# Optimization experiments

Hardware: AMD Instinct MI355X
Metric: run time of the kernel (lower is better)

Reference implementation:

```python
import jax, jax.numpy as jnp
import numpy as np


def _d2(a, b):
    # squared euclidean distances, clamped at 0 (matches _full_cdist before sqrt)
    a2 = jnp.sum(a * a, axis=1)[:, None]
    b2 = jnp.sum(b * b, axis=1)[None, :]
    return jnp.clip(a2 + b2 - 2.0 * (a @ b.T), 0.0, None)


def _node_weights(pts, w1, b1, w2, b2):
    h = jax.nn.relu(pts @ w1 + b1)
    logits = h @ w2 + b2
    w = jax.nn.softplus(logits) + 1e-6
    w = w / jnp.sum(w)
    return w[:, 0]


def setup_inputs() -> dict:
    key = jax.random.key(0)
    ks = jax.random.split(key, 8)
    N, M, D, H, S = 8192, 8192, 2, 32, 3
    return {
        "base_points": jax.random.normal(ks[0], (N, D), jnp.float32),
        "target_points": jax.random.normal(ks[1], (M, D), jnp.float32),
        "log_sigmas": jnp.log(jnp.array([0.05, 0.1, 0.2], jnp.float32)),
        "log_scale": 0.1 * jax.random.normal(ks[2], (D,), jnp.float32),
        "wn_w1": jax.random.normal(ks[3], (D, H), jnp.float32) / np.sqrt(D),
        "wn_b1": jnp.zeros((H,), jnp.float32),
        "wn_w2": jax.random.normal(ks[4], (H, 1), jnp.float32) / np.sqrt(H),
        "wn_b2": jnp.zeros((1,), jnp.float32),
        "g_w1": jax.random.normal(ks[5], (4, H), jnp.float32) / 2.0,
        "g_b1": jnp.zeros((H,), jnp.float32),
        "g_w2": jax.random.normal(ks[6], (H, S), jnp.float32) / np.sqrt(H),
        "g_b2": jnp.zeros((S,), jnp.float32),
        "bias": jnp.zeros((1,), jnp.float32),
    }


def reference(base_points, target_points, log_sigmas, log_scale,
              wn_w1, wn_b1, wn_w2, wn_b2,
              g_w1, g_b1, g_w2, g_b2, bias):
    # learned anisotropic per-axis scale
    scale = jnp.exp(log_scale)
    base = base_points * scale
    target = target_points * scale

    # learned positive, normalized node weights (shared weight_net)
    w_b = _node_weights(base, wn_w1, wn_b1, wn_w2, wn_b2)
    w_t = _node_weights(target, wn_w1, wn_b1, wn_w2, wn_b2)

    # kde_mmd_loss with center=True: subtract weighted mean of each cloud.
    bc = base - jnp.sum(w_b[:, None] * base, axis=0)
    tc = target - jnp.sum(w_t[:, None] * target, axis=0)

    # squared distances computed ONCE, reused across all sigma bands
    d2_aa = _d2(bc, bc)
    d2_bb = _d2(tc, tc)
    d2_ab = _d2(bc, tc)

    sigmas = jnp.exp(log_sigmas)

    def band_loss(sigma):
        inv = 1.0 / (2.0 * sigma * sigma)
        kaa = jnp.exp(-d2_aa * inv)
        kbb = jnp.exp(-d2_bb * inv)
        kab = jnp.exp(-d2_ab * inv)
        # weighted MMD^2: w_a K_aa w_a + w_b K_bb w_b - 2 w_a K_ab w_b
        return (w_b @ (kaa @ w_b) + w_t @ (kbb @ w_t)
                - 2.0 * (w_b @ (kab @ w_t)))

    per_band = jnp.stack([band_loss(sigmas[i]) for i in range(sigmas.shape[0])])

    # gating statistics (torch.tensor([...]) detaches -> stop_gradient)
    dist = jnp.sqrt(_d2(base, target))
    mean_dist = jnp.mean(dist)
    var_dist = jnp.var(dist, ddof=1)  # torch .var() is unbiased
    n_base = base_points.shape[0]
    size_diff = abs(float(n_base - target_points.shape[0])) / (n_base + 1e-6)
    weight_var = jnp.var(w_b, ddof=1) + jnp.var(w_t, ddof=1)
    stats = jax.lax.stop_gradient(
        jnp.stack([mean_dist, var_dist,
                   jnp.asarray(size_diff, base.dtype), weight_var]))

    mix_logits = jax.nn.relu(stats @ g_w1 + g_b1) @ g_w2 + g_b2
    gw = jax.nn.softplus(mix_logits)
    gw = gw / jnp.sum(gw)
    return jnp.sum(gw * per_band) + bias[0]
```

## Files before the change

kernel.cpp:

```cpp
#include <hip/hip_runtime.h>
#include <math.h>

#define JT 64
#define ITILE 1024
#define T8 8
#define NJOB_AB 1024
#define NJOB_TRI 576
#define NBLK (NJOB_AB + 2 * NJOB_TRI)
#define L2E 1.4426950408889634f

typedef float v2f __attribute__((ext_vector_type(2)));

__device__ inline float fexp2n(float x) {
  float r;
  asm("v_exp_f32 %0, -%1" : "=v"(r) : "v"(x));
  return r;
}
__device__ inline float fsqrt(float x) {
  float r;
  asm("v_sqrt_f32 %0, %1" : "=v"(r) : "v"(x));
  return r;
}
__device__ inline v2f pk_add(v2f a, v2f b) {
  v2f d;
  asm("v_pk_add_f32 %0, %1, %2" : "=v"(d) : "v"(a), "v"(b));
  return d;
}
__device__ inline v2f pk_mul(v2f a, v2f b) {
  v2f d;
  asm("v_pk_mul_f32 %0, %1, %2" : "=v"(d) : "v"(a), "v"(b));
  return d;
}
__device__ inline v2f pk_fma(v2f a, v2f b, v2f c) {
  v2f d;
  asm("v_pk_fma_f32 %0, %1, %2, %3" : "=v"(d) : "v"(a), "v"(b), "v"(c));
  return d;
}

__device__ inline double wred_d(double v) {
#pragma unroll
  for (int o = 32; o > 0; o >>= 1) v += __shfl_down(v, o, 64);
  return v;
}

__device__ inline double bred(double v, double* sm) {
  v = wred_d(v);
  __syncthreads();
  if ((threadIdx.x & 63) == 0) sm[threadIdx.x >> 6] = v;
  __syncthreads();
  return sm[0] + sm[1] + sm[2] + sm[3];
}

__device__ inline void slot_reduce(const double* slot, double* smean) {
  if (threadIdx.x < 64) {
    int l = threadIdx.x;
    const double* sl = slot + l * 8;
#pragma unroll
    for (int c = 0; c < 7; ++c) {
      double v = sl[c];
      double vb = (l < 32) ? v : 0.0;
      double vt = (l < 32) ? 0.0 : v;
      vb = wred_d(vb);
      vt = wred_d(vt);
      if (l == 0) {
        smean[c] = vb;
        smean[8 + c] = vt;
      }
    }
  }
}

__global__ __launch_bounds__(256) void prep_kernel(
    const float* __restrict__ base, const float* __restrict__ target,
    const float* __restrict__ log_sigmas, const float* __restrict__ log_scale,
    const float* __restrict__ w1, const float* __restrict__ b1,
    const float* __restrict__ w2, const float* __restrict__ b2,
    float4* __restrict__ pxyu, double* __restrict__ slot,
    unsigned* __restrict__ fctr, int n) {
  __shared__ double sm[4];
  int gid = blockIdx.x * 256 + threadIdx.x;
  int isT = gid >= n;
  const float* pts = isT ? target : base;
  int idx = isT ? gid - n : gid;
  float ex = __expf(log_scale[0]);
  float ey = __expf(log_scale[1]);
  float s2 = __expf(log_sigmas[2]);
  float r2 = __fsqrt_rn(L2E / (2.f * s2 * s2));
  float2 p = ((const float2*)pts)[idx];
  float xr = p.x * ex, yr = p.y * ey;
  float logit = b2[0];
#pragma unroll
  for (int k = 0; k < 32; ++k) {
    float h = fmaf(xr, w1[k], fmaf(yr, w1[32 + k], b1[k]));
    h = fmaxf(h, 0.f);
    logit = fmaf(h, w2[k], logit);
  }
  float u = fmaxf(logit, 0.f) + log1pf(__expf(-fabsf(logit))) + 1e-6f;
  float X = xr * r2, Y = yr * r2;
  float q = fmaf(X, X, Y * Y);
  pxyu[gid] = make_float4(X, Y, q, u);
  double su = bred((double)u, sm);
  double qu = bred((double)u * (double)u, sm);
  double mx = bred((double)u * (double)X, sm);
  double my = bred((double)u * (double)Y, sm);
  double sx = bred((double)X, sm);
  double sy = bred((double)Y, sm);
  double sq = bred((double)q, sm);
  if (threadIdx.x == 0) {
    double* s = slot + blockIdx.x * 8;
    s[0] = su;
    s[1] = qu;
    s[2] = mx;
    s[3] = my;
    s[4] = sx;
    s[5] = sy;
    s[6] = sq;
    if (blockIdx.x == 0) *fctr = 0u;
  }
}

template <bool AB>
__device__ inline void tile_loop_fast(const float* sx, const float* sy,
                                      const float* su, const float* snb,
                                      const v2f vnxi[4], const v2f vnyi[4],
                                      const v2f vali[4], v2f a0[4], v2f a1[4],
                                      v2f a2[4], float& sdo) {
  float sdl = 0.f, sdh = 0.f;
#pragma unroll 2
  for (int jj = 0; jj < JT / 2; ++jj) {
    v2f vxj = *(const v2f*)&sx[2 * jj];
    v2f vyj = *(const v2f*)&sy[2 * jj];
    v2f vuj = *(const v2f*)&su[2 * jj];
    v2f vnbj;
    if constexpr (AB) vnbj = *(const v2f*)&snb[2 * jj];
#pragma unroll
    for (int i = 0; i < 4; ++i) {
      v2f dx = pk_add(vxj, vnxi[i]);
      v2f dy = pk_add(vyj, vnyi[i]);
      v2f t = pk_mul(dx, dx);
      v2f pos = pk_fma(dy, dy, t);
      float k2l = fexp2n(pos.x);
      float k2h = fexp2n(pos.y);
      v2f k2 = {k2l, k2h};
      v2f t2 = pk_mul(k2, k2);
      v2f k1 = pk_mul(t2, t2);
      v2f t4 = pk_mul(k1, k1);
      v2f k0 = pk_mul(t4, t4);
      a0[i] = pk_fma(vuj, k0, a0[i]);
      a1[i] = pk_fma(vuj, k1, a1[i]);
      a2[i] = pk_fma(vuj, k2, a2[i]);
      if constexpr (AB) {
        v2f d2u = pk_add(pk_add(pos, vali[i]), vnbj);
        sdl += fsqrt(fmaxf(d2u.x, 0.f));
        sdh += fsqrt(fmaxf(d2u.y, 0.f));
      }
    }
  }
  sdo = sdl + sdh;
}

__global__ __launch_bounds__(256) void pair_kernel(
    const float4* __restrict__ pxyu, const double* __restrict__ slot,
    double* __restrict__ paa, double* __restrict__ pbb,
    double* __restrict__ pab, double* __restrict__ psd,
    unsigned* __restrict__ fctr, const float* __restrict__ log_sigmas,
    const float* __restrict__ g_w1, const float* __restrict__ g_b1,
    const float* __restrict__ g_w2, const float* __restrict__ g_b2,
    const float* __restrict__ bias, float* __restrict__ out, int n) {
  __shared__ __align__(16) float sx[JT];
  __shared__ __align__(16) float sy[JT];
  __shared__ __align__(16) float su[JT];
  __shared__ __align__(16) float snb[JT];
  __shared__ double sm[4];
  __shared__ double smean[16];
  __shared__ int lastf;

  int b = blockIdx.x;
  int tid = threadIdx.x;
  int m, it, jt = 0, j0, pidx;
  if (b < NJOB_AB) {
    m = 2;
    pidx = b;
    it = b >> 7;
    j0 = (b & 127) * JT;
  } else {
    int r = b - NJOB_AB;
    m = (r < NJOB_TRI) ? 0 : 1;
    if (m == 1) r -= NJOB_TRI;
    pidx = r;
    int tile = r >> 4;
    int q = r & 15;
    int idx = tile, len = T8;
    it = 0;
    while (idx >= len) {
      idx -= len;
      --len;
      ++it;
    }
    jt = it + idx;
    j0 = jt * ITILE + q * JT;
  }
  const float4* pI = pxyu + ((m == 1) ? n : 0);
  const float4* pJ = pxyu + ((m == 0) ? 0 : n);

  float cx = 0.f, cy = 0.f, cx2 = 0.f, cy2 = 0.f, cc = 0.f;
  if (m == 2) {
    slot_reduce(slot, smean);
  }

  float s0 = __expf(log_sigmas[0]);
  float s1 = __expf(log_sigmas[1]);
  float s2 = __expf(log_sigmas[2]);
  float rr0 = (s2 * s2) / (s0 * s0);
  float rr1 = (s2 * s2) / (s1 * s1);
  bool fast = (fabsf(rr0 - 16.f) <= 0.016f) && (fabsf(rr1 - 4.f) <= 0.004f);

  if (m == 2) {
    __syncthreads();
    cx = (float)(smean[2] / smean[0] - smean[10] / smean[8]);
    cy = (float)(smean[3] / smean[0] - smean[11] / smean[8]);
    cx2 = 2.f * cx;
    cy2 = 2.f * cy;
    cc = cx * cx + cy * cy;
  }

  if (tid < JT) {
    float4 v = pJ[j0 + tid];
    sx[tid] = v.x;
    sy[tid] = v.y;
    su[tid] = v.w;
    if (m == 2) snb[tid] = -fmaf(cx2, v.x, cy2 * v.y);
  }
  __syncthreads();

  int i0 = it * ITILE + tid;
  v2f vnxi[4], vnyi[4], vali[4];
  float u[4];
#pragma unroll
  for (int i = 0; i < 4; ++i) {
    float4 P = pI[i0 + i * 256];
    u[i] = P.w;
    float xv = P.x, yv = P.y, alv = 0.f;
    if (m == 2) {
      xv -= cx;
      yv -= cy;
      alv = fmaf(cx2, xv, cy2 * yv) + cc;
    }
    vnxi[i] = (v2f){-xv, -xv};
    vnyi[i] = (v2f){-yv, -yv};
    vali[i] = (v2f){alv, alv};
  }

  v2f a0[4] = {}, a1[4] = {}, a2[4] = {};
  float sd = 0.f;
  if (fast) {
    if (m == 2)
      tile_loop_fast<true>(sx, sy, su, snb, vnxi, vnyi, vali, a0, a1, a2, sd);
    else
      tile_loop_fast<false>(sx, sy, su, snb, vnxi, vnyi, vali, a0, a1, a2,
                            sd);
  } else {
    for (int j = 0; j < JT; ++j) {
      float xj = sx[j], yj = sy[j], uj = su[j];
#pragma unroll
      for (int i = 0; i < 4; ++i) {
        float dx = xj + vnxi[i].x;
        float dy = yj + vnyi[i].x;
        float pos = fmaf(dx, dx, dy * dy);
        float k2 = fexp2n(pos);
        float k1 = fexp2n(pos * rr1);
        float k0 = fexp2n(pos * rr0);
        a0[i].x = fmaf(uj, k0, a0[i].x);
        a1[i].x = fmaf(uj, k1, a1[i].x);
        a2[i].x = fmaf(uj, k2, a2[i].x);
        if (m == 2) {
          float d2u = fmaxf(pos + vali[i].x + snb[j], 0.f);
          sd += fsqrt(d2u);
        }
      }
    }
  }

  double wgt = (m != 2 && jt != it) ? 2.0 : 1.0;
  double c0 = 0.0, c1 = 0.0, c2 = 0.0;
#pragma unroll
  for (int i = 0; i < 4; ++i) {
    c0 += (double)u[i] * (double)(a0[i].x + a0[i].y);
    c1 += (double)u[i] * (double)(a1[i].x + a1[i].y);
    c2 += (double)u[i] * (double)(a2[i].x + a2[i].y);
  }
  double r0 = bred(c0, sm) * wgt;
  double r1 = bred(c1, sm) * wgt;
  double r2d = bred(c2, sm) * wgt;
  double* prow = (m == 0) ? paa : (m == 1) ? pbb : pab;
  int stride = (m == 2) ? NJOB_AB : NJOB_TRI;
  if (tid == 0) {
    prow[0 * stride + pidx] = r0;
    prow[1 * stride + pidx] = r1;
    prow[2 * stride + pidx] = r2d;
  }
  if (m == 2) {
    double rsd = bred((double)sd, sm);
    if (tid == 0) psd[pidx] = rsd;
  }

  if (tid == 0) {
    __threadfence();
    unsigned old = atomicAdd(fctr, 1u);
    lastf = (old == NBLK - 1) ? 1 : 0;
  }
  __syncthreads();
  if (!lastf) return;
  __threadfence();

  slot_reduce(slot, smean);
  __syncthreads();
  int t = tid;
  double vaa[3], vbb[3], vab[3];
  for (int s = 0; s < 3; ++s) {
    const double* pa = paa + s * NJOB_TRI;
    const double* pb = pbb + s * NJOB_TRI;
    const double* pc = pab + s * NJOB_AB;
    double va = pa[t] + pa[t + 256] + ((t < 64) ? pa[t + 512] : 0.0);
    double vb = pb[t] + pb[t + 256] + ((t < 64) ? pb[t + 512] : 0.0);
    double vc = pc[t] + pc[t + 256] + pc[t + 512] + pc[t + 768];
    vaa[s] = bred(va, sm);
    vbb[s] = bred(vb, sm);
    vab[s] = bred(vc, sm);
  }
  double sdt = bred(psd[t] + psd[t + 256] + psd[t + 512] + psd[t + 768], sm);

  if (tid == 0) {
    double Sb = smean[0], Qb = smean[1], St = smean[8], Qt = smean[9];
    double SxB = smean[4], SyB = smean[5], SqB = smean[6];
    double SxT = smean[12], SyT = smean[13], SqT = smean[14];
    double pband[3];
    for (int s = 0; s < 3; ++s)
      pband[s] = vaa[s] / (Sb * Sb) + vbb[s] / (St * St) -
                 2.0 * vab[s] / (Sb * St);
    double s2d = (double)s2;
    double r2sq = (double)L2E / (2.0 * s2d * s2d);
    double NN = (double)n;
    double sq_scaled = NN * (SqB + SqT) - 2.0 * (SxB * SxT + SyB * SyT);
    double sd_real = sdt / sqrt(r2sq);
    double sq_real = sq_scaled / r2sq;
    double NM = NN * NN;
    double mean_d = sd_real / NM;
    double var_d = (sq_real - sd_real * sd_real / NM) / (NM - 1.0);
    double wv = (Qb / (Sb * Sb) - 1.0 / NN) / (NN - 1.0) +
                (Qt / (St * St) - 1.0 / NN) / (NN - 1.0);
    float st[4] = {(float)mean_d, (float)var_d, 0.f, (float)wv};
    float gl[3] = {g_b2[0], g_b2[1], g_b2[2]};
    for (int k = 0; k < 32; ++k) {
      float h = g_b1[k];
      for (int c = 0; c < 4; ++c) h = fmaf(st[c], g_w1[c * 32 + k], h);
      h = fmaxf(h, 0.f);
      for (int s = 0; s < 3; ++s) gl[s] = fmaf(h, g_w2[k * 3 + s], gl[s]);
    }
    float gw[3];
    float gsum = 0.f;
    for (int s = 0; s < 3; ++s) {
      gw[s] = fmaxf(gl[s], 0.f) + log1pf(__expf(-fabsf(gl[s])));
      gsum += gw[s];
    }
    double r = 0.0;
    for (int s = 0; s < 3; ++s) r += (double)(gw[s] / gsum) * pband[s];
    out[0] = (float)(r + (double)bias[0]);
  }
}

extern "C" void kernel_launch(void* const* d_in, const int* in_sizes, int n_in,
                              void* d_out, int out_size, void* d_ws,
                              size_t ws_size, hipStream_t stream) {
  const float* base = (const float*)d_in[0];
  const float* target = (const float*)d_in[1];
  const float* log_sigmas = (const float*)d_in[2];
  const float* log_scale = (const float*)d_in[3];
  const float* wn_w1 = (const float*)d_in[4];
  const float* wn_b1 = (const float*)d_in[5];
  const float* wn_w2 = (const float*)d_in[6];
  const float* wn_b2 = (const float*)d_in[7];
  const float* g_w1 = (const float*)d_in[8];
  const float* g_b1 = (const float*)d_in[9];
  const float* g_w2 = (const float*)d_in[10];
  const float* g_b2 = (const float*)d_in[11];
  const float* bias = (const float*)d_in[12];
  int n = in_sizes[0] / 2;

  double* dbase = (double*)d_ws;
  double* slot = dbase;
  double* paa = dbase + 512;
  double* pbb = paa + 3 * NJOB_TRI;
  double* pab = pbb + 3 * NJOB_TRI;
  double* psd = pab + 3 * NJOB_AB;
  double* dend = psd + NJOB_AB;
  float4* pxyu = (float4*)dend;
  unsigned* fctr = (unsigned*)(pxyu + 2 * n);

  prep_kernel<<<(2 * n) / 256, 256, 0, stream>>>(
      base, target, log_sigmas, log_scale, wn_w1, wn_b1, wn_w2, wn_b2, pxyu,
      slot, fctr, n);
  pair_kernel<<<NBLK, 256, 0, stream>>>(pxyu, slot, paa, pbb, pab, psd, fctr,
                                        log_sigmas, g_w1, g_b1, g_w2, g_b2,
                                        bias, (float*)d_out, n);
}
```

Before: 155.8 us.

## Map lanes to j points and stream i points through wave-uniform scalar loads

Each lane now holds one j point in registers, and each wave walks a quarter of the 1024-point i tile. The i points are loaded with a wave-uniform index, so they can become scalar/broadcast loads, which removes the LDS staging tile and its barrier. The distance is expanded algebraically as 2*xi*xj + 2*yi*yj - qi - qj, with -q stored in the prep buffer, so each pair costs fewer ops. The packed-f32 inline asm is dropped for scalar code, and the cdist term is rebuilt from the negated argument. This adds per-iteration global loads and may lose precision through the expansion.

```diff
diff --git a/kernel.cpp b/kernel.cpp
--- a/kernel.cpp
+++ b/kernel.cpp
@@ -9,32 +9,15 @@
 #define NBLK (NJOB_AB + 2 * NJOB_TRI)
 #define L2E 1.4426950408889634f
 
-typedef float v2f __attribute__((ext_vector_type(2)));
-
-__device__ inline float fexp2n(float x) {
+__device__ inline float fexp2(float x) {
   float r;
-  asm("v_exp_f32 %0, -%1" : "=v"(r) : "v"(x));
+  asm("v_exp_f32 %0, %1" : "=v"(r) : "v"(x));
   return r;
 }
 __device__ inline float fsqrt(float x) {
   float r;
   asm("v_sqrt_f32 %0, %1" : "=v"(r) : "v"(x));
   return r;
-}
-__device__ inline v2f pk_add(v2f a, v2f b) {
-  v2f d;
-  asm("v_pk_add_f32 %0, %1, %2" : "=v"(d) : "v"(a), "v"(b));
-  return d;
-}
-__device__ inline v2f pk_mul(v2f a, v2f b) {
-  v2f d;
-  asm("v_pk_mul_f32 %0, %1, %2" : "=v"(d) : "v"(a), "v"(b));
-  return d;
-}
-__device__ inline v2f pk_fma(v2f a, v2f b, v2f c) {
-  v2f d;
-  asm("v_pk_fma_f32 %0, %1, %2, %3" : "=v"(d) : "v"(a), "v"(b), "v"(c));
-  return d;
 }
 
 __device__ inline double wred_d(double v) {
@@ -98,7 +81,7 @@
   float u = fmaxf(logit, 0.f) + log1pf(__expf(-fabsf(logit))) + 1e-6f;
   float X = xr * r2, Y = yr * r2;
   float q = fmaf(X, X, Y * Y);
-  pxyu[gid] = make_float4(X, Y, q, u);
+  pxyu[gid] = make_float4(X, Y, -q, u);
   double su = bred((double)u, sm);
   double qu = bred((double)u * (double)u, sm);
   double mx = bred((double)u * (double)X, sm);
@@ -119,44 +102,42 @@
   }
 }
 
-template <bool AB>
-__device__ inline void tile_loop_fast(const float* sx, const float* sy,
-                                      const float* su, const float* snb,
-                                      const v2f vnxi[4], const v2f vnyi[4],
-                                      const v2f vali[4], v2f a0[4], v2f a1[4],
-                                      v2f a2[4], float& sdo) {
-  float sdl = 0.f, sdh = 0.f;
-#pragma unroll 2
-  for (int jj = 0; jj < JT / 2; ++jj) {
-    v2f vxj = *(const v2f*)&sx[2 * jj];
-    v2f vyj = *(const v2f*)&sy[2 * jj];
-    v2f vuj = *(const v2f*)&su[2 * jj];
-    v2f vnbj;
-    if constexpr (AB) vnbj = *(const v2f*)&snb[2 * jj];
-#pragma unroll
-    for (int i = 0; i < 4; ++i) {
-      v2f dx = pk_add(vxj, vnxi[i]);
-      v2f dy = pk_add(vyj, vnyi[i]);
-      v2f t = pk_mul(dx, dx);
-      v2f pos = pk_fma(dy, dy, t);
-      float k2l = fexp2n(pos.x);
-      float k2h = fexp2n(pos.y);
-      v2f k2 = {k2l, k2h};
-      v2f t2 = pk_mul(k2, k2);
-      v2f k1 = pk_mul(t2, t2);
-      v2f t4 = pk_mul(k1, k1);
-      v2f k0 = pk_mul(t4, t4);
-      a0[i] = pk_fma(vuj, k0, a0[i]);
-      a1[i] = pk_fma(vuj, k1, a1[i]);
-      a2[i] = pk_fma(vuj, k2, a2[i]);
-      if constexpr (AB) {
-        v2f d2u = pk_add(pk_add(pos, vali[i]), vnbj);
-        sdl += fsqrt(fmaxf(d2u.x, 0.f));
-        sdh += fsqrt(fmaxf(d2u.y, 0.f));
-      }
-    }
-  }
-  sdo = sdl + sdh;
+template <bool AB, bool FAST>
+__device__ inline void iloop(const float4* __restrict__ pI, int ibase,
+                             float xj2, float yj2, float mqj, float nhj,
+                             float cx2, float cy2, float cc, float rr0,
+                             float rr1, float a[3], float& sd) {
+#pragma unroll 8
+  for (int ii = 0; ii < ITILE / 4; ++ii) {
+    float4 I = pI[ibase + ii];
+    float t = fmaf(I.y, yj2, mqj);
+    float narg = fmaf(I.x, xj2, t) + I.z;
+    float karg;
+    if constexpr (AB) {
+      float ngi = fmaf(cx2, I.x, fmaf(cy2, I.y, -cc));
+      karg = (narg + ngi) + nhj;
+    } else {
+      karg = narg;
+    }
+    float k2 = fexp2(karg);
+    float k0, k1;
+    if constexpr (FAST) {
+      float t2 = k2 * k2;
+      k1 = t2 * t2;
+      float t4 = k1 * k1;
+      k0 = t4 * t4;
+    } else {
+      k1 = fexp2(karg * rr1);
+      k0 = fexp2(karg * rr0);
+    }
+    a[0] = fmaf(I.w, k0, a[0]);
+    a[1] = fmaf(I.w, k1, a[1]);
+    a[2] = fmaf(I.w, k2, a[2]);
+    if constexpr (AB) {
+      float d2u = fmaxf(-narg, 0.f);
+      sd += fsqrt(d2u);
+    }
+  }
 }
 
 __global__ __launch_bounds__(256) void pair_kernel(
@@ -167,10 +148,6 @@
     const float* __restrict__ g_w1, const float* __restrict__ g_b1,
     const float* __restrict__ g_w2, const float* __restrict__ g_b2,
     const float* __restrict__ bias, float* __restrict__ out, int n) {
-  __shared__ __align__(16) float sx[JT];
-  __shared__ __align__(16) float sy[JT];
-  __shared__ __align__(16) float su[JT];
-  __shared__ __align__(16) float snb[JT];
   __shared__ double sm[4];
   __shared__ double smean[16];
   __shared__ int lastf;
@@ -203,7 +180,6 @@
   const float4* pI = pxyu + ((m == 1) ? n : 0);
   const float4* pJ = pxyu + ((m == 0) ? 0 : n);
 
-  float cx = 0.f, cy = 0.f, cx2 = 0.f, cy2 = 0.f, cc = 0.f;
   if (m == 2) {
     slot_reduce(slot, smean);
   }
@@ -215,83 +191,49 @@
   float rr1 = (s2 * s2) / (s1 * s1);
   bool fast = (fabsf(rr0 - 16.f) <= 0.016f) && (fabsf(rr1 - 4.f) <= 0.004f);
 
+  float cx2 = 0.f, cy2 = 0.f, cc = 0.f;
   if (m == 2) {
     __syncthreads();
-    cx = (float)(smean[2] / smean[0] - smean[10] / smean[8]);
-    cy = (float)(smean[3] / smean[0] - smean[11] / smean[8]);
+    float cx = (float)(smean[2] / smean[0] - smean[10] / smean[8]);
+    float cy = (float)(smean[3] / smean[0] - smean[11] / smean[8]);
     cx2 = 2.f * cx;
     cy2 = 2.f * cy;
     cc = cx * cx + cy * cy;
   }
 
-  if (tid < JT) {
-    float4 v = pJ[j0 + tid];
-    sx[tid] = v.x;
-    sy[tid] = v.y;
-    su[tid] = v.w;
-    if (m == 2) snb[tid] = -fmaf(cx2, v.x, cy2 * v.y);
-  }
-  __syncthreads();
-
-  int i0 = it * ITILE + tid;
-  v2f vnxi[4], vnyi[4], vali[4];
-  float u[4];
-#pragma unroll
-  for (int i = 0; i < 4; ++i) {
-    float4 P = pI[i0 + i * 256];
-    u[i] = P.w;
-    float xv = P.x, yv = P.y, alv = 0.f;
-    if (m == 2) {
-      xv -= cx;
-      yv -= cy;
-      alv = fmaf(cx2, xv, cy2 * yv) + cc;
-    }
-    vnxi[i] = (v2f){-xv, -xv};
-    vnyi[i] = (v2f){-yv, -yv};
-    vali[i] = (v2f){alv, alv};
-  }
-
-  v2f a0[4] = {}, a1[4] = {}, a2[4] = {};
+  float4 J = pJ[j0 + (tid & 63)];
+  float xj2 = J.x + J.x;
+  float yj2 = J.y + J.y;
+  float mqj = J.z;
+  float uj = J.w;
+  float nhj = 0.f;
+  if (m == 2) nhj = -fmaf(cx2, J.x, cy2 * J.y);
+
+  int wid = __builtin_amdgcn_readfirstlane(tid >> 6);
+  int ibase = it * ITILE + wid * (ITILE / 4);
+
+  float a[3] = {0.f, 0.f, 0.f};
   float sd = 0.f;
-  if (fast) {
-    if (m == 2)
-      tile_loop_fast<true>(sx, sy, su, snb, vnxi, vnyi, vali, a0, a1, a2, sd);
+  if (m == 2) {
+    if (fast)
+      iloop<true, true>(pI, ibase, xj2, yj2, mqj, nhj, cx2, cy2, cc, rr0, rr1,
+                        a, sd);
     else
-      tile_loop_fast<false>(sx, sy, su, snb, vnxi, vnyi, vali, a0, a1, a2,
-                            sd);
+      iloop<true, false>(pI, ibase, xj2, yj2, mqj, nhj, cx2, cy2, cc, rr0,
+                         rr1, a, sd);
   } else {
-    for (int j = 0; j < JT; ++j) {
-      float xj = sx[j], yj = sy[j], uj = su[j];
-#pragma unroll
-      for (int i = 0; i < 4; ++i) {
-        float dx = xj + vnxi[i].x;
-        float dy = yj + vnyi[i].x;
-        float pos = fmaf(dx, dx, dy * dy);
-        float k2 = fexp2n(pos);
-        float k1 = fexp2n(pos * rr1);
-        float k0 = fexp2n(pos * rr0);
-        a0[i].x = fmaf(uj, k0, a0[i].x);
-        a1[i].x = fmaf(uj, k1, a1[i].x);
-        a2[i].x = fmaf(uj, k2, a2[i].x);
-        if (m == 2) {
-          float d2u = fmaxf(pos + vali[i].x + snb[j], 0.f);
-          sd += fsqrt(d2u);
-        }
-      }
-    }
+    if (fast)
+      iloop<false, true>(pI, ibase, xj2, yj2, mqj, nhj, cx2, cy2, cc, rr0,
+                         rr1, a, sd);
+    else
+      iloop<false, false>(pI, ibase, xj2, yj2, mqj, nhj, cx2, cy2, cc, rr0,
+                          rr1, a, sd);
   }
 
   double wgt = (m != 2 && jt != it) ? 2.0 : 1.0;
-  double c0 = 0.0, c1 = 0.0, c2 = 0.0;
-#pragma unroll
-  for (int i = 0; i < 4; ++i) {
-    c0 += (double)u[i] * (double)(a0[i].x + a0[i].y);
-    c1 += (double)u[i] * (double)(a1[i].x + a1[i].y);
-    c2 += (double)u[i] * (double)(a2[i].x + a2[i].y);
-  }
-  double r0 = bred(c0, sm) * wgt;
-  double r1 = bred(c1, sm) * wgt;
-  double r2d = bred(c2, sm) * wgt;
+  double r0 = bred((double)(uj * a[0]), sm) * wgt;
+  double r1 = bred((double)(uj * a[1]), sm) * wgt;
+  double r2d = bred((double)(uj * a[2]), sm) * wgt;
   double* prow = (m == 0) ? paa : (m == 1) ? pbb : pab;
   int stride = (m == 2) ? NJOB_AB : NJOB_TRI;
   if (tid == 0) {
```

Measured after the change: 176.9 us. 13.6% more time.
